# Kernel optimization log

Hardware: AMD Instinct MI355X
Metric: run time of the kernel (lower is better)

The kernel has to match this reference:

```python
import jax, jax.numpy as jnp
import numpy as np


def setup_inputs() -> dict:
    key = jax.random.key(0)
    ks = jax.random.split(key, 5)
    b, t, q_dim, kv_dim, h = 16, 128, 256, 64, 4
    c = t - 1
    q_x = jax.random.normal(ks[0], (b, t, q_dim), dtype=jnp.float32)
    kv_x = jax.random.normal(ks[1], (b, t, c, kv_dim), dtype=jnp.float32)
    # Linear weights stored as [in, out]; no biases (bias=False in torch module).
    sq = 1.0 / np.sqrt(q_dim)
    sk = 1.0 / np.sqrt(kv_dim)
    Wq = jax.random.uniform(ks[2], (q_dim, kv_dim * h), jnp.float32, -sq, sq)
    Wk = jax.random.uniform(ks[3], (kv_dim, kv_dim * h), jnp.float32, -sk, sk)
    Wv = jax.random.uniform(ks[4], (kv_dim, kv_dim * h), jnp.float32, -sk, sk)
    return {"q_x": q_x, "kv_x": kv_x, "Wq": Wq, "Wk": Wk, "Wv": Wv}


def reference(q_x, kv_x, Wq, Wk, Wv):
    b, t, c, k = kv_x.shape  # c = t - 1
    h = Wq.shape[1] // k
    # projections
    q = (q_x @ Wq).reshape(b, t, h, k)          # [b,t,h,k]
    keys = (kv_x @ Wk).reshape(b, t, c, h, k)   # [b,t,c,h,k]
    vals = (kv_x @ Wv).reshape(b, t, c, h, k)
    # per-token attention over the c-sized context
    scores = jnp.einsum('bthk,btchk->bthc', q, keys) / jnp.sqrt(jnp.float32(k))
    w = jax.nn.softmax(scores, axis=-1)          # softmax over context dim
    out = jnp.einsum('bthc,btchk->bthk', w, vals)
    return out.reshape(b, t, h * k)
```

## Files before the change

kernel.cpp:

```cpp
#include <hip/hip_runtime.h>
#include <math.h>

#define Bdim 16
#define Tdim 128
#define Cdim 127
#define Hdim 4
#define QD   256
#define HK   256
#define BT   (Bdim * Tdim)

__global__ __launch_bounds__(256) void qk_fused(
        const float* __restrict__ q_x,
        const float* __restrict__ Wq,
        const float* __restrict__ Wk,
        float* __restrict__ qk) {
    __shared__ __align__(16) float q_s[4][256];
    __shared__ __align__(16) float p_s[4][4][68];
    int RB = blockIdx.x;
    int tid = threadIdx.x;
    {
        int r = tid >> 6, kq = tid & 63;
        *(float4*)&q_s[r][kq*4] =
            *(const float4*)(q_x + (size_t)(RB*4 + r) * QD + kq * 4);
    }
    __syncthreads();

    float acc[4] = {0.f, 0.f, 0.f, 0.f};
    #pragma unroll 4
    for (int i4 = 0; i4 < 64; ++i4) {
        float w0 = Wq[(size_t)(4*i4+0) * HK + tid];
        float w1 = Wq[(size_t)(4*i4+1) * HK + tid];
        float w2 = Wq[(size_t)(4*i4+2) * HK + tid];
        float w3 = Wq[(size_t)(4*i4+3) * HK + tid];
        #pragma unroll
        for (int r = 0; r < 4; ++r) {
            float4 qv = *(const float4*)&q_s[r][i4*4];
            acc[r] = fmaf(qv.x, w0, fmaf(qv.y, w1, fmaf(qv.z, w2, fmaf(qv.w, w3, acc[r]))));
        }
    }
    int h = tid >> 6, m = tid & 63;
    #pragma unroll
    for (int r = 0; r < 4; ++r) p_s[r][h][m] = acc[r];
    __syncthreads();

    const float4* wk4 = (const float4*)(Wk + (size_t)m * HK + h * 64);
    float4 wkr[16];
    #pragma unroll
    for (int j = 0; j < 16; ++j) wkr[j] = wk4[j];
    float a2[4] = {0.f, 0.f, 0.f, 0.f};
    #pragma unroll
    for (int j4 = 0; j4 < 16; ++j4) {
        #pragma unroll
        for (int r = 0; r < 4; ++r) {
            float4 pv = *(const float4*)&p_s[r][h][j4*4];
            a2[r] = fmaf(pv.x, wkr[j4].x, fmaf(pv.y, wkr[j4].y,
                    fmaf(pv.z, wkr[j4].z, fmaf(pv.w, wkr[j4].w, a2[r]))));
        }
    }
    #pragma unroll
    for (int r = 0; r < 4; ++r)
        qk[(size_t)(RB*4 + r) * HK + tid] = a2[r];
}

__global__ __launch_bounds__(256, 2) void attn_core(
        const float* __restrict__ kv_x,
        const float* __restrict__ qk_g,
        float* __restrict__ wx_buf,
        float* __restrict__ denom_buf) {
    __shared__ __align__(16) float qk_s[4][4][68];

    int tid = threadIdx.x;
    int wv = tid >> 6, lane = tid & 63;
    int bt = blockIdx.x * 4 + wv;
    int g = lane & 3;
    int r = lane >> 2;
    const float* Xr = kv_x + (size_t)bt * (Cdim * 64);

    {
        int h = lane >> 4, j4 = lane & 15;
        *(float4*)&qk_s[wv][h][j4 * 4] =
            *(const float4*)(qk_g + (size_t)bt * HK + lane * 4);
    }

    float4 V[16];
    #pragma unroll
    for (int j = 0; j < 16; ++j) V[j] = make_float4(0.f, 0.f, 0.f, 0.f);
    float dsum = 0.f;

    #pragma unroll
    for (int k = 0; k < 8; ++k) {
        int c = r + 16 * k;
        bool valid = (c < Cdim);
        const float4* xr = (const float4*)(Xr + (valid ? c : 0) * 64);
        float4 R[16];
        #pragma unroll
        for (int j = 0; j < 16; ++j) R[j] = xr[j];
        float s = 0.f;
        #pragma unroll
        for (int j = 0; j < 16; ++j) {
            float4 q = *(const float4*)&qk_s[wv][g][j * 4];
            s = fmaf(q.x, R[j].x, fmaf(q.y, R[j].y,
                fmaf(q.z, R[j].z, fmaf(q.w, R[j].w, s))));
        }
        float e = valid ? __expf(s * 0.125f) : 0.f;
        dsum += e;
        #pragma unroll
        for (int j = 0; j < 16; ++j) {
            V[j].x = fmaf(e, R[j].x, V[j].x);
            V[j].y = fmaf(e, R[j].y, V[j].y);
            V[j].z = fmaf(e, R[j].z, V[j].z);
            V[j].w = fmaf(e, R[j].w, V[j].w);
        }
    }

    #pragma unroll
    for (int m = 4; m <= 32; m <<= 1) {
        #pragma unroll
        for (int j = 0; j < 16; ++j) {
            V[j].x += __shfl_xor(V[j].x, m, 64);
            V[j].y += __shfl_xor(V[j].y, m, 64);
            V[j].z += __shfl_xor(V[j].z, m, 64);
            V[j].w += __shfl_xor(V[j].w, m, 64);
        }
        dsum += __shfl_xor(dsum, m, 64);
    }

    if (r == 0) {
        float4* w = (float4*)(wx_buf + (size_t)bt * HK + g * 64);
        #pragma unroll
        for (int j = 0; j < 16; ++j) w[j] = V[j];
        denom_buf[(size_t)bt * 4 + g] = dsum;
    }
}

__global__ __launch_bounds__(256) void vproj(
        const float* __restrict__ wx_buf,
        const float* __restrict__ denom_buf,
        const float* __restrict__ Wv,
        float* __restrict__ out) {
    __shared__ __align__(16) float4 wx_s[4][64];
    __shared__ __align__(16) float4 dn_s[4];
    int B0 = blockIdx.x * 4;
    int tid = threadIdx.x;
    {
        int r = tid >> 6, l = tid & 63;
        wx_s[r][l] = ((const float4*)(wx_buf + (size_t)(B0 + r) * HK))[l];
    }
    if (tid < 4) dn_s[tid] = *(const float4*)(denom_buf + (size_t)(B0 + tid) * 4);
    __syncthreads();

    int h = tid >> 6;
    float wvr[64];
    #pragma unroll
    for (int j = 0; j < 64; ++j) wvr[j] = Wv[(size_t)j * HK + tid];
    #pragma unroll
    for (int r = 0; r < 4; ++r) {
        float acc = 0.f;
        #pragma unroll
        for (int j4 = 0; j4 < 16; ++j4) {
            float4 w4 = wx_s[r][h * 16 + j4];
            acc = fmaf(w4.x, wvr[j4*4+0], fmaf(w4.y, wvr[j4*4+1],
                  fmaf(w4.z, wvr[j4*4+2], fmaf(w4.w, wvr[j4*4+3], acc))));
        }
        float4 dn = dn_s[r];
        float d = (h == 0) ? dn.x : (h == 1) ? dn.y : (h == 2) ? dn.z : dn.w;
        out[(size_t)(B0 + r) * HK + tid] = acc / d;
    }
}

extern "C" void kernel_launch(void* const* d_in, const int* in_sizes, int n_in,
                              void* d_out, int out_size, void* d_ws, size_t ws_size,
                              hipStream_t stream) {
    const float* q_x  = (const float*)d_in[0];
    const float* kv_x = (const float*)d_in[1];
    const float* Wq   = (const float*)d_in[2];
    const float* Wk   = (const float*)d_in[3];
    const float* Wv   = (const float*)d_in[4];
    float* out = (float*)d_out;

    float* qk    = (float*)d_ws;
    float* wxb   = qk + (size_t)BT * HK;
    float* denom = wxb + (size_t)BT * HK;

    qk_fused <<<BT / 4, 256, 0, stream>>>(q_x, Wq, Wk, qk);
    attn_core<<<BT / 4, 256, 0, stream>>>(kv_x, qk, wxb, denom);
    vproj    <<<BT / 4, 256, 0, stream>>>(wxb, denom, Wv, out);
}
```

Baseline: 40.77 us.

## Split attention row dot-product across 4 lanes with DPP reduction to cut registers

Reorganises attn_core so each row of kv_x is split across four lanes (each handling 16 of the 64 channels), with the partial scores combined via DPP xor-swaps instead of one lane owning the full 64-wide row. Q is held in registers rather than shared memory, and the register footprint drops from 64-float accumulators plus 64-float row buffers to 16 each, allowing launch bounds of 6 blocks per SM for more memory-level parallelism. The trade is more loop iterations (32 instead of 8), with each lane loading 64-byte chunks rather than full 256-byte rows, plus extra DPP ops per row.

```diff
diff --git a/kernel.cpp b/kernel.cpp
--- a/kernel.cpp
+++ b/kernel.cpp
@@ -8,6 +8,14 @@
 #define QD   256
 #define HK   256
 #define BT   (Bdim * Tdim)
+
+#define DPP_XOR1 0xB1
+#define DPP_XOR2 0x4E
+template<int CTRL>
+__device__ __forceinline__ float dpp_movf(float x) {
+    return __int_as_float(__builtin_amdgcn_update_dpp(
+        0, __float_as_int(x), CTRL, 0xF, 0xF, true));
+}
 
 __global__ __launch_bounds__(256) void qk_fused(
         const float* __restrict__ q_x,
@@ -62,74 +70,71 @@
         qk[(size_t)(RB*4 + r) * HK + tid] = a2[r];
 }
 
-__global__ __launch_bounds__(256, 2) void attn_core(
+__global__ __launch_bounds__(256, 6) void attn_core(
         const float* __restrict__ kv_x,
         const float* __restrict__ qk_g,
         float* __restrict__ wx_buf,
         float* __restrict__ denom_buf) {
-    __shared__ __align__(16) float qk_s[4][4][68];
-
     int tid = threadIdx.x;
     int wv = tid >> 6, lane = tid & 63;
     int bt = blockIdx.x * 4 + wv;
-    int g = lane & 3;
-    int r = lane >> 2;
+    int r  = lane >> 4;
+    int g  = (lane >> 2) & 3;
+    int jq = lane & 3;
     const float* Xr = kv_x + (size_t)bt * (Cdim * 64);
 
-    {
-        int h = lane >> 4, j4 = lane & 15;
-        *(float4*)&qk_s[wv][h][j4 * 4] =
-            *(const float4*)(qk_g + (size_t)bt * HK + lane * 4);
-    }
+    const float4* qkp = (const float4*)(qk_g + (size_t)bt * HK + g * 64 + jq * 16);
+    float4 Q0 = qkp[0], Q1 = qkp[1], Q2 = qkp[2], Q3 = qkp[3];
 
-    float4 V[16];
-    #pragma unroll
-    for (int j = 0; j < 16; ++j) V[j] = make_float4(0.f, 0.f, 0.f, 0.f);
+    float4 V0 = {0,0,0,0}, V1 = {0,0,0,0}, V2 = {0,0,0,0}, V3 = {0,0,0,0};
     float dsum = 0.f;
 
-    #pragma unroll
-    for (int k = 0; k < 8; ++k) {
-        int c = r + 16 * k;
+    #pragma unroll 2
+    for (int k = 0; k < 32; ++k) {
+        int c = r + 4 * k;
         bool valid = (c < Cdim);
-        const float4* xr = (const float4*)(Xr + (valid ? c : 0) * 64);
-        float4 R[16];
-        #pragma unroll
-        for (int j = 0; j < 16; ++j) R[j] = xr[j];
-        float s = 0.f;
-        #pragma unroll
-        for (int j = 0; j < 16; ++j) {
-            float4 q = *(const float4*)&qk_s[wv][g][j * 4];
-            s = fmaf(q.x, R[j].x, fmaf(q.y, R[j].y,
-                fmaf(q.z, R[j].z, fmaf(q.w, R[j].w, s))));
-        }
+        const float4* xr = (const float4*)(Xr + (valid ? c : 0) * 64) + jq * 4;
+        float4 R0 = xr[0], R1 = xr[1], R2 = xr[2], R3 = xr[3];
+        float s;
+        s = fmaf(Q0.x, R0.x, Q0.y * R0.y);
+        s = fmaf(Q0.z, R0.z, fmaf(Q0.w, R0.w, s));
+        s = fmaf(Q1.x, R1.x, fmaf(Q1.y, R1.y, s));
+        s = fmaf(Q1.z, R1.z, fmaf(Q1.w, R1.w, s));
+        s = fmaf(Q2.x, R2.x, fmaf(Q2.y, R2.y, s));
+        s = fmaf(Q2.z, R2.z, fmaf(Q2.w, R2.w, s));
+        s = fmaf(Q3.x, R3.x, fmaf(Q3.y, R3.y, s));
+        s = fmaf(Q3.z, R3.z, fmaf(Q3.w, R3.w, s));
+        s += dpp_movf<DPP_XOR1>(s);
+        s += dpp_movf<DPP_XOR2>(s);
         float e = valid ? __expf(s * 0.125f) : 0.f;
         dsum += e;
-        #pragma unroll
-        for (int j = 0; j < 16; ++j) {
-            V[j].x = fmaf(e, R[j].x, V[j].x);
-            V[j].y = fmaf(e, R[j].y, V[j].y);
-            V[j].z = fmaf(e, R[j].z, V[j].z);
-            V[j].w = fmaf(e, R[j].w, V[j].w);
-        }
+        V0.x = fmaf(e, R0.x, V0.x); V0.y = fmaf(e, R0.y, V0.y);
+        V0.z = fmaf(e, R0.z, V0.z); V0.w = fmaf(e, R0.w, V0.w);
+        V1.x = fmaf(e, R1.x, V1.x); V1.y = fmaf(e, R1.y, V1.y);
+        V1.z = fmaf(e, R1.z, V1.z); V1.w = fmaf(e, R1.w, V1.w);
+        V2.x = fmaf(e, R2.x, V2.x); V2.y = fmaf(e, R2.y, V2.y);
+        V2.z = fmaf(e, R2.z, V2.z); V2.w = fmaf(e, R2.w, V2.w);
+        V3.x = fmaf(e, R3.x, V3.x); V3.y = fmaf(e, R3.y, V3.y);
+        V3.z = fmaf(e, R3.z, V3.z); V3.w = fmaf(e, R3.w, V3.w);
     }
 
     #pragma unroll
-    for (int m = 4; m <= 32; m <<= 1) {
-        #pragma unroll
-        for (int j = 0; j < 16; ++j) {
-            V[j].x += __shfl_xor(V[j].x, m, 64);
-            V[j].y += __shfl_xor(V[j].y, m, 64);
-            V[j].z += __shfl_xor(V[j].z, m, 64);
-            V[j].w += __shfl_xor(V[j].w, m, 64);
-        }
+    for (int m = 16; m <= 32; m <<= 1) {
+        V0.x += __shfl_xor(V0.x, m, 64); V0.y += __shfl_xor(V0.y, m, 64);
+        V0.z += __shfl_xor(V0.z, m, 64); V0.w += __shfl_xor(V0.w, m, 64);
+        V1.x += __shfl_xor(V1.x, m, 64); V1.y += __shfl_xor(V1.y, m, 64);
+        V1.z += __shfl_xor(V1.z, m, 64); V1.w += __shfl_xor(V1.w, m, 64);
+        V2.x += __shfl_xor(V2.x, m, 64); V2.y += __shfl_xor(V2.y, m, 64);
+        V2.z += __shfl_xor(V2.z, m, 64); V2.w += __shfl_xor(V2.w, m, 64);
+        V3.x += __shfl_xor(V3.x, m, 64); V3.y += __shfl_xor(V3.y, m, 64);
+        V3.z += __shfl_xor(V3.z, m, 64); V3.w += __shfl_xor(V3.w, m, 64);
         dsum += __shfl_xor(dsum, m, 64);
     }
 
     if (r == 0) {
-        float4* w = (float4*)(wx_buf + (size_t)bt * HK + g * 64);
-        #pragma unroll
-        for (int j = 0; j < 16; ++j) w[j] = V[j];
-        denom_buf[(size_t)bt * 4 + g] = dsum;
+        float4* w = (float4*)(wx_buf + (size_t)bt * HK + g * 64 + jq * 16);
+        w[0] = V0; w[1] = V1; w[2] = V2; w[3] = V3;
+        if (jq == 0) denom_buf[(size_t)bt * 4 + g] = dsum;
     }
 }
 
```

Result: no change. 40.18 us (-1.5%).

## Restructure attn_core lane mapping with register-resident Q, DPP score reduction, and transpose-reduce

Applied to the files above, without the earlier changes.

Each lane of attn_core now owns a 16-float slice of the 64-wide kv row across all 4 heads, instead of a whole row for a single head. Q is held in registers rather than LDS, and partial dot products are combined with DPP xor moves within groups of four lanes. The row loads are software-pipelined with double buffering. The final reduction becomes a butterfly transpose-reduce, so every lane writes one float4 instead of shuffling 64 values. The aim is to cut redundant reads of kv_x (each row was previously read by four lanes), shuffle traffic and register pressure. The cost is extra select logic and dependence on DPP.

```diff
diff --git a/kernel.cpp b/kernel.cpp
--- a/kernel.cpp
+++ b/kernel.cpp
@@ -8,6 +8,32 @@
 #define QD   256
 #define HK   256
 #define BT   (Bdim * Tdim)
+
+#define DPP_XOR1 0xB1
+#define DPP_XOR2 0x4E
+template<int CTRL>
+__device__ __forceinline__ float dpp_movf(float x) {
+    return __int_as_float(__builtin_amdgcn_update_dpp(
+        0, __float_as_int(x), CTRL, 0xF, 0xF, true));
+}
+__device__ __forceinline__ float dot4(float4 a, float4 b, float s) {
+    return fmaf(a.x, b.x, fmaf(a.y, b.y, fmaf(a.z, b.z, fmaf(a.w, b.w, s))));
+}
+__device__ __forceinline__ float4 fma4(float e, float4 x, float4 v) {
+    v.x = fmaf(e, x.x, v.x); v.y = fmaf(e, x.y, v.y);
+    v.z = fmaf(e, x.z, v.z); v.w = fmaf(e, x.w, v.w);
+    return v;
+}
+__device__ __forceinline__ float4 add4(float4 a, float4 b) {
+    return make_float4(a.x + b.x, a.y + b.y, a.z + b.z, a.w + b.w);
+}
+__device__ __forceinline__ float4 shfl4(float4 v, int m) {
+    return make_float4(__shfl_xor(v.x, m, 64), __shfl_xor(v.y, m, 64),
+                       __shfl_xor(v.z, m, 64), __shfl_xor(v.w, m, 64));
+}
+__device__ __forceinline__ float4 sel4(int c, float4 a, float4 b) {
+    return c ? a : b;
+}
 
 __global__ __launch_bounds__(256) void qk_fused(
         const float* __restrict__ q_x,
@@ -67,70 +93,114 @@
         const float* __restrict__ qk_g,
         float* __restrict__ wx_buf,
         float* __restrict__ denom_buf) {
-    __shared__ __align__(16) float qk_s[4][4][68];
-
     int tid = threadIdx.x;
     int wv = tid >> 6, lane = tid & 63;
     int bt = blockIdx.x * 4 + wv;
-    int g = lane & 3;
-    int r = lane >> 2;
+    int r  = lane >> 2;
+    int jq = lane & 3;
     const float* Xr = kv_x + (size_t)bt * (Cdim * 64);
 
-    {
-        int h = lane >> 4, j4 = lane & 15;
-        *(float4*)&qk_s[wv][h][j4 * 4] =
-            *(const float4*)(qk_g + (size_t)bt * HK + lane * 4);
-    }
-
-    float4 V[16];
-    #pragma unroll
-    for (int j = 0; j < 16; ++j) V[j] = make_float4(0.f, 0.f, 0.f, 0.f);
-    float dsum = 0.f;
-
-    #pragma unroll
-    for (int k = 0; k < 8; ++k) {
-        int c = r + 16 * k;
-        bool valid = (c < Cdim);
-        const float4* xr = (const float4*)(Xr + (valid ? c : 0) * 64);
-        float4 R[16];
-        #pragma unroll
-        for (int j = 0; j < 16; ++j) R[j] = xr[j];
-        float s = 0.f;
-        #pragma unroll
-        for (int j = 0; j < 16; ++j) {
-            float4 q = *(const float4*)&qk_s[wv][g][j * 4];
-            s = fmaf(q.x, R[j].x, fmaf(q.y, R[j].y,
-                fmaf(q.z, R[j].z, fmaf(q.w, R[j].w, s))));
-        }
-        float e = valid ? __expf(s * 0.125f) : 0.f;
-        dsum += e;
-        #pragma unroll
-        for (int j = 0; j < 16; ++j) {
-            V[j].x = fmaf(e, R[j].x, V[j].x);
-            V[j].y = fmaf(e, R[j].y, V[j].y);
-            V[j].z = fmaf(e, R[j].z, V[j].z);
-            V[j].w = fmaf(e, R[j].w, V[j].w);
-        }
-    }
+    const float4* qb = (const float4*)(qk_g + (size_t)bt * HK);
+    float4 Q00 = qb[ 0 + jq*4 + 0], Q01 = qb[ 0 + jq*4 + 1],
+           Q02 = qb[ 0 + jq*4 + 2], Q03 = qb[ 0 + jq*4 + 3];
+    float4 Q10 = qb[16 + jq*4 + 0], Q11 = qb[16 + jq*4 + 1],
+           Q12 = qb[16 + jq*4 + 2], Q13 = qb[16 + jq*4 + 3];
+    float4 Q20 = qb[32 + jq*4 + 0], Q21 = qb[32 + jq*4 + 1],
+           Q22 = qb[32 + jq*4 + 2], Q23 = qb[32 + jq*4 + 3];
+    float4 Q30 = qb[48 + jq*4 + 0], Q31 = qb[48 + jq*4 + 1],
+           Q32 = qb[48 + jq*4 + 2], Q33 = qb[48 + jq*4 + 3];
+
+    float4 V00={0,0,0,0},V01={0,0,0,0},V02={0,0,0,0},V03={0,0,0,0};
+    float4 V10={0,0,0,0},V11={0,0,0,0},V12={0,0,0,0},V13={0,0,0,0};
+    float4 V20={0,0,0,0},V21={0,0,0,0},V22={0,0,0,0},V23={0,0,0,0};
+    float4 V30={0,0,0,0},V31={0,0,0,0},V32={0,0,0,0},V33={0,0,0,0};
+    float d0=0.f, d1=0.f, d2=0.f, d3=0.f;
+    float4 A0, A1, A2, A3, B0, B1, B2, B3;
+
+#define LOADR(P0,P1,P2,P3,KK) do {                                           \
+    int c_ = 16*(KK) + r;                                                    \
+    const float4* xp_ = (const float4*)(Xr + (size_t)((c_ < Cdim) ? c_ : 0)  \
+                                        * 64) + jq * 4;                      \
+    P0 = xp_[0]; P1 = xp_[1]; P2 = xp_[2]; P3 = xp_[3];                      \
+} while (0)
+
+#define COMP(P0,P1,P2,P3,KK) do {                                            \
+    float s0 = dot4(Q00,P0,0.f); s0 = dot4(Q01,P1,s0);                       \
+    s0 = dot4(Q02,P2,s0); s0 = dot4(Q03,P3,s0);                              \
+    float s1 = dot4(Q10,P0,0.f); s1 = dot4(Q11,P1,s1);                       \
+    s1 = dot4(Q12,P2,s1); s1 = dot4(Q13,P3,s1);                              \
+    float s2 = dot4(Q20,P0,0.f); s2 = dot4(Q21,P1,s2);                       \
+    s2 = dot4(Q22,P2,s2); s2 = dot4(Q23,P3,s2);                              \
+    float s3 = dot4(Q30,P0,0.f); s3 = dot4(Q31,P1,s3);                       \
+    s3 = dot4(Q32,P2,s3); s3 = dot4(Q33,P3,s3);                              \
+    s0 += dpp_movf<DPP_XOR1>(s0); s0 += dpp_movf<DPP_XOR2>(s0);              \
+    s1 += dpp_movf<DPP_XOR1>(s1); s1 += dpp_movf<DPP_XOR2>(s1);              \
+    s2 += dpp_movf<DPP_XOR1>(s2); s2 += dpp_movf<DPP_XOR2>(s2);              \
+    s3 += dpp_movf<DPP_XOR1>(s3); s3 += dpp_movf<DPP_XOR2>(s3);              \
+    bool vld_ = (16*(KK) + r) < Cdim;                                        \
+    float e0 = vld_ ? __expf(s0 * 0.125f) : 0.f;                             \
+    float e1 = vld_ ? __expf(s1 * 0.125f) : 0.f;                             \
+    float e2 = vld_ ? __expf(s2 * 0.125f) : 0.f;                             \
+    float e3 = vld_ ? __expf(s3 * 0.125f) : 0.f;                             \
+    d0 += e0; d1 += e1; d2 += e2; d3 += e3;                                  \
+    V00=fma4(e0,P0,V00); V01=fma4(e0,P1,V01);                                \
+    V02=fma4(e0,P2,V02); V03=fma4(e0,P3,V03);                                \
+    V10=fma4(e1,P0,V10); V11=fma4(e1,P1,V11);                                \
+    V12=fma4(e1,P2,V12); V13=fma4(e1,P3,V13);                                \
+    V20=fma4(e2,P0,V20); V21=fma4(e2,P1,V21);                                \
+    V22=fma4(e2,P2,V22); V23=fma4(e2,P3,V23);                                \
+    V30=fma4(e3,P0,V30); V31=fma4(e3,P1,V31);                                \
+    V32=fma4(e3,P2,V32); V33=fma4(e3,P3,V33);                                \
+} while (0)
+
+    LOADR(A0,A1,A2,A3,0);
+    LOADR(B0,B1,B2,B3,1);
+    COMP (A0,A1,A2,A3,0);
+    LOADR(A0,A1,A2,A3,2);
+    COMP (B0,B1,B2,B3,1);
+    LOADR(B0,B1,B2,B3,3);
+    COMP (A0,A1,A2,A3,2);
+    LOADR(A0,A1,A2,A3,4);
+    COMP (B0,B1,B2,B3,3);
+    LOADR(B0,B1,B2,B3,5);
+    COMP (A0,A1,A2,A3,4);
+    LOADR(A0,A1,A2,A3,6);
+    COMP (B0,B1,B2,B3,5);
+    LOADR(B0,B1,B2,B3,7);
+    COMP (A0,A1,A2,A3,6);
+    COMP (B0,B1,B2,B3,7);
+#undef LOADR
+#undef COMP
+
+    int r0 = (lane >> 2) & 1, r1 = (lane >> 3) & 1;
+    int r2 = (lane >> 4) & 1, r3 = (lane >> 5) & 1;
+    float4 K00 = add4(sel4(r0, V01, V00), shfl4(sel4(r0, V00, V01), 4));
+    float4 K01 = add4(sel4(r0, V03, V02), shfl4(sel4(r0, V02, V03), 4));
+    float4 K10 = add4(sel4(r0, V11, V10), shfl4(sel4(r0, V10, V11), 4));
+    float4 K11 = add4(sel4(r0, V13, V12), shfl4(sel4(r0, V12, V13), 4));
+    float4 K20 = add4(sel4(r0, V21, V20), shfl4(sel4(r0, V20, V21), 4));
+    float4 K21 = add4(sel4(r0, V23, V22), shfl4(sel4(r0, V22, V23), 4));
+    float4 K30 = add4(sel4(r0, V31, V30), shfl4(sel4(r0, V30, V31), 4));
+    float4 K31 = add4(sel4(r0, V33, V32), shfl4(sel4(r0, V32, V33), 4));
+    float4 L0 = add4(sel4(r1, K01, K00), shfl4(sel4(r1, K00, K01), 8));
+    float4 L1 = add4(sel4(r1, K11, K10), shfl4(sel4(r1, K10, K11), 8));
+    float4 L2 = add4(sel4(r1, K21, K20), shfl4(sel4(r1, K20, K21), 8));
+    float4 L3 = add4(sel4(r1, K31, K30), shfl4(sel4(r1, K30, K31), 8));
+    float4 M0 = add4(sel4(r2, L1, L0), shfl4(sel4(r2, L0, L1), 16));
+    float4 M1 = add4(sel4(r2, L3, L2), shfl4(sel4(r2, L2, L3), 16));
+    float4 F = add4(sel4(r3, M1, M0), shfl4(sel4(r3, M0, M1), 32));
 
     #pragma unroll
     for (int m = 4; m <= 32; m <<= 1) {
-        #pragma unroll
-        for (int j = 0; j < 16; ++j) {
-            V[j].x += __shfl_xor(V[j].x, m, 64);
-            V[j].y += __shfl_xor(V[j].y, m, 64);
-            V[j].z += __shfl_xor(V[j].z, m, 64);
-            V[j].w += __shfl_xor(V[j].w, m, 64);
-        }
-        dsum += __shfl_xor(dsum, m, 64);
-    }
-
-    if (r == 0) {
-        float4* w = (float4*)(wx_buf + (size_t)bt * HK + g * 64);
-        #pragma unroll
-        for (int j = 0; j < 16; ++j) w[j] = V[j];
-        denom_buf[(size_t)bt * 4 + g] = dsum;
-    }
+        d0 += __shfl_xor(d0, m, 64); d1 += __shfl_xor(d1, m, 64);
+        d2 += __shfl_xor(d2, m, 64); d3 += __shfl_xor(d3, m, 64);
+    }
+
+    int H  = (r3 << 1) | r2;
+    int qo = (r1 << 1) | r0;
+    ((float4*)(wx_buf + (size_t)bt * HK))[H * 16 + jq * 4 + qo] = F;
+    if (lane == 0)
+        *(float4*)(denom_buf + (size_t)bt * 4) = make_float4(d0, d1, d2, d3);
 }
 
 __global__ __launch_bounds__(256) void vproj(
```

After: 36.50 us. 1.12x faster.
